# Performance work log

Hardware: AMD Instinct MI355X
Metric: run time of the kernel (lower is better)

## Reference

```python
import jax, jax.numpy as jnp
import numpy as np

B, S, D = 8, 1024, 768
H = 12
HD = D // H  # 64
SCALE = 1.0 / (HD ** 0.5)


def setup_inputs() -> dict:
    key = jax.random.key(0)
    ks = jax.random.split(key, 5)
    x = jax.random.normal(ks[0], (B, S, D), dtype=jnp.float32)
    W_qkv = jax.random.normal(ks[1], (D, 3 * D), dtype=jnp.float32) * 0.02
    b_qkv = jax.random.normal(ks[2], (3 * D,), dtype=jnp.float32) * 0.02
    W_proj = jax.random.normal(ks[3], (D, D), dtype=jnp.float32) * 0.02
    b_proj = jax.random.normal(ks[4], (D,), dtype=jnp.float32) * 0.02
    return {"x": x, "W_qkv": W_qkv, "b_qkv": b_qkv, "W_proj": W_proj, "b_proj": b_proj}


def reference(x, W_qkv, b_qkv, W_proj, b_proj):
    b, s, d = x.shape
    # QKV projection: (B, S, 3D) -> (3, B, H, S, HD)
    qkv = x @ W_qkv + b_qkv
    qkv = qkv.reshape(b, s, 3, H, HD).transpose(2, 0, 3, 1, 4)
    q, k, v = qkv[0], qkv[1], qkv[2]
    # scaled dot-product attention (full matrix, as in the original)
    scores = jnp.einsum("bhqd,bhkd->bhqk", q, k) * SCALE
    attn = jax.nn.softmax(scores, axis=-1)
    out = jnp.einsum("bhqk,bhkd->bhqd", attn, v)
    # merge heads: (B, S, D)
    out = out.transpose(0, 2, 1, 3).reshape(b, s, d)
    return out @ W_proj + b_proj
```

## Files before the change

kernel.cpp:

```cpp
#include <hip/hip_runtime.h>
#include <math.h>

typedef __attribute__((ext_vector_type(8))) unsigned short ushortx8;
typedef __attribute__((ext_vector_type(8))) __bf16 bf16x8;
typedef __attribute__((ext_vector_type(4))) float floatx4;
typedef __attribute__((ext_vector_type(16))) float floatx16;

#define NH 12
#define SEQ 1024
#define DM 768
#define HD 64
#define GK 768
#define QK_SCALE 0.18033688011112042f

#define GLDS16(gp, lp) __builtin_amdgcn_global_load_lds( \
    (const __attribute__((address_space(1))) unsigned int*)(const void*)(gp), \
    (__attribute__((address_space(3))) unsigned int*)(lp), 16, 0, 0)

__device__ __forceinline__ unsigned short f2bf(float f) {
    union { float f; unsigned u; } v; v.f = f;
    unsigned r = v.u + 0x7fffu + ((v.u >> 16) & 1u);
    return (unsigned short)(r >> 16);
}

__device__ __forceinline__ unsigned pk2bf(float f0, float f1) {
    union { float f; unsigned u; } a, b; a.f = f0; b.f = f1;
    return ((a.u + 0x8000u) >> 16) | ((b.u + 0x8000u) & 0xffff0000u);
}

__device__ __forceinline__ float fast_exp2(float x) {
    float r;
    asm("v_exp_f32 %0, %1" : "=v"(r) : "v"(x));
    return r;
}

__global__ void k_prep(const float* __restrict__ x, unsigned short* __restrict__ x_bf,
                       const float* __restrict__ Wqkv, unsigned short* __restrict__ WqkvT,
                       const float* __restrict__ Wproj, unsigned short* __restrict__ WprojT) {
    __shared__ float tile[32][33];
    int bx = blockIdx.x;
    if (bx < 6144) {
        int i = bx * 256 + threadIdx.x;
        float4 v = ((const float4*)x)[i];
        ushort4 o;
        o.x = f2bf(v.x); o.y = f2bf(v.y); o.z = f2bf(v.z); o.w = f2bf(v.w);
        ((ushort4*)x_bf)[i] = o;
        return;
    }
    const float* in; unsigned short* out; int R, C, c0, r0;
    if (bx < 7872) {
        int t = bx - 6144;
        in = Wqkv; out = WqkvT; R = 768; C = 2304;
        c0 = (t % 72) * 32; r0 = (t / 72) * 32;
    } else {
        int t = bx - 7872;
        in = Wproj; out = WprojT; R = 768; C = 768;
        c0 = (t % 24) * 32; r0 = (t / 24) * 32;
    }
    int tx = threadIdx.x & 31, ty = threadIdx.x >> 5;
#pragma unroll
    for (int i = 0; i < 4; i++)
        tile[ty + 8 * i][tx] = in[(size_t)(r0 + ty + 8 * i) * C + c0 + tx];
    __syncthreads();
#pragma unroll
    for (int i = 0; i < 4; i++)
        out[(size_t)(c0 + ty + 8 * i) * R + r0 + tx] = f2bf(tile[tx][ty + 8 * i]);
}

__device__ __forceinline__ void stage6(const unsigned short* gA, const unsigned short* gB,
                                       unsigned short* lbuf, int w, int k0) {
#pragma unroll
    for (int g = 0; g < 4; g++)
        GLDS16(gA + (size_t)(w * 64 + g * 16) * GK + k0, lbuf + (w * 64 + g * 16) * 32);
#pragma unroll
    for (int g = 0; g < 2; g++)
        GLDS16(gB + (size_t)(w * 32 + g * 16) * GK + k0, lbuf + 8192 + (w * 32 + g * 16) * 32);
}

__device__ __forceinline__ void mfma24(const unsigned short* Ab, const unsigned short* Bb,
                                       int wm, int wn, int l15, int csw,
                                       floatx4 (&acc)[8][3]) {
    bf16x8 af[8], bfr[3];
#pragma unroll
    for (int m = 0; m < 8; m++)
        af[m] = __builtin_bit_cast(bf16x8,
            *(const ushortx8*)&Ab[(wm * 128 + m * 16 + l15) * 32 + csw]);
#pragma unroll
    for (int n = 0; n < 3; n++)
        bfr[n] = __builtin_bit_cast(bf16x8,
            *(const ushortx8*)&Bb[(wn * 48 + n * 16 + l15) * 32 + csw]);
#pragma unroll
    for (int m = 0; m < 8; m++)
#pragma unroll
        for (int n = 0; n < 3; n++)
            acc[m][n] = __builtin_amdgcn_mfma_f32_16x16x32_bf16(af[m], bfr[n], acc[m][n], 0, 0, 0);
}

__device__ __forceinline__ void gemm_mainloop(const unsigned short* __restrict__ A,
                                              const unsigned short* __restrict__ Bt,
                                              unsigned short* smem, int m0, int n0,
                                              int w, int lane, floatx4 (&acc)[8][3]) {
    int quad = lane >> 4, l15 = lane & 15;
    int wm = w >> 1, wn = w & 1;
    int rA = lane >> 2;
    int cSwz = ((lane & 3) ^ ((lane >> 3) & 3)) * 8;
    int csw = (quad ^ ((l15 >> 1) & 3)) * 8;
    const unsigned short* gA = A + (size_t)(m0 + rA) * GK + cSwz;
    const unsigned short* gB = Bt + (size_t)(n0 + rA) * GK + cSwz;

    stage6(gA, gB, smem, w, 0);
    stage6(gA, gB, smem + 12288, w, 32);
#pragma unroll 1
    for (int t = 0; t < 24; t++) {
        if (t < 23) asm volatile("s_waitcnt vmcnt(6)" ::: "memory");
        else        asm volatile("s_waitcnt vmcnt(0)" ::: "memory");
        __builtin_amdgcn_s_barrier();
        asm volatile("" ::: "memory");
        const unsigned short* Ab = smem + (t & 1) * 12288;
        __builtin_amdgcn_s_setprio(1);
        mfma24(Ab, Ab + 8192, wm, wn, l15, csw, acc);
        __builtin_amdgcn_s_setprio(0);
        asm volatile("" ::: "memory");
        __builtin_amdgcn_s_barrier();
        asm volatile("" ::: "memory");
        if (t < 22) stage6(gA, gB, smem + (t & 1) * 12288, w, (t + 2) * 32);
    }
}

__global__ __launch_bounds__(256, 3) void k_gemm_qkv(
    const unsigned short* __restrict__ A, const unsigned short* __restrict__ Bt,
    const float* __restrict__ bias,
    unsigned short* __restrict__ Qb, unsigned short* __restrict__ Kb,
    unsigned short* __restrict__ Vt) {
    __shared__ unsigned short smem[25344];
    int tid = threadIdx.x;
    int w = tid >> 6, lane = tid & 63;
    int quad = lane >> 4, l15 = lane & 15;
    int wm = w >> 1, wn = w & 1;
    int lin = blockIdx.x;
    int xcd = lin & 7, slot = lin >> 3;
    int mt_i = xcd * 4 + (slot & 3);
    int nt_i = slot >> 2;
    int m0 = mt_i * 256, n0 = nt_i * 96;

    floatx4 acc[8][3] = {};
    gemm_mainloop(A, Bt, smem, m0, n0, w, lane, acc);

    int tsel = nt_i / 8;
    int bb = m0 >> 10;
    int s_base0 = (m0 & 1023) + wm * 128;
    if (tsel < 2) {
        unsigned short* __restrict__ dst = (tsel == 0) ? Qb : Kb;
#pragma unroll
        for (int m = 0; m < 8; m++) {
            int s_base = s_base0 + m * 16 + quad * 4;
#pragma unroll
            for (int n = 0; n < 3; n++) {
                int n_g = n0 + wn * 48 + n * 16 + l15;
                int nloc = n_g - tsel * 768;
                int hh = nloc >> 6, dd = nloc & 63;
                float bv = bias[n_g];
                size_t base = ((size_t)(bb * NH + hh) * SEQ + s_base) * HD + dd;
                if (tsel == 0) {
#pragma unroll
                    for (int rg = 0; rg < 4; rg++)
                        dst[base + (size_t)rg * HD] = f2bf((acc[m][n][rg] + bv) * QK_SCALE);
                } else {
#pragma unroll
                    for (int rg = 0; rg < 4; rg++)
                        dst[base + (size_t)rg * HD] = f2bf(acc[m][n][rg] + bv);
                }
            }
        }
    } else {
        __syncthreads();
#pragma unroll
        for (int m = 0; m < 8; m++) {
#pragma unroll
            for (int n = 0; n < 3; n++) {
                int col = wn * 48 + n * 16 + l15;
                float bv = bias[n0 + col];
                ushort4 pk;
                pk.x = f2bf(acc[m][n][0] + bv);
                pk.y = f2bf(acc[m][n][1] + bv);
                pk.z = f2bf(acc[m][n][2] + bv);
                pk.w = f2bf(acc[m][n][3] + bv);
                *(ushort4*)&smem[col * 264 + wm * 128 + m * 16 + quad * 4] = pk;
            }
        }
        __syncthreads();
        if (tid < 192) {
            int col = tid >> 1, part = tid & 1;
            int dglob = (n0 - 1536) + col;
            int hh = dglob >> 6, dd = dglob & 63;
            size_t gbase = ((size_t)(bb * NH + hh) * HD + dd) * SEQ + (m0 & 1023) + part * 128;
#pragma unroll
            for (int i = 0; i < 16; i++)
                *(uint4*)&Vt[gbase + i * 8] = *(const uint4*)&smem[col * 264 + part * 128 + i * 8];
        }
    }
}

__global__ __launch_bounds__(256) void k_attn(
    const unsigned short* __restrict__ Qb, const unsigned short* __restrict__ Kb,
    const unsigned short* __restrict__ Vt, unsigned short* __restrict__ attn_out) {
    __shared__ unsigned short Ks[2][64 * 64];
    __shared__ unsigned short Vts[2][64 * 64];
    __shared__ unsigned short Pt[4][32 * 72];
    int tid = threadIdx.x;
    int w = tid >> 6, lane = tid & 63;
    int l31 = lane & 31, lh = lane >> 5;
    int lin = blockIdx.x;
    int xcd = lin & 7, slot = lin >> 3;
    int bh = xcd * 12 + (slot >> 3);
    int qt = slot & 7;
    int b = bh / NH, h = bh - b * NH;
    const unsigned short* Qp = Qb + (size_t)bh * SEQ * HD;
    const unsigned short* Kp = Kb + (size_t)bh * SEQ * HD;
    const unsigned short* Vp = Vt + (size_t)bh * HD * SEQ;
    int q0w = qt * 128 + w * 32;
    unsigned short* Ptw = &Pt[w][0];

    bf16x8 qf[4];
#pragma unroll
    for (int ds = 0; ds < 4; ds++)
        qf[ds] = __builtin_bit_cast(bf16x8,
            *(const ushortx8*)&Qp[(size_t)(q0w + l31) * HD + ds * 16 + lh * 8]);

    floatx16 o[2] = {};
    float lsum = 0.f;

    int rr = tid >> 3, cc8 = (tid & 7) * 8;
    int cs = cc8 ^ ((rr & 7) * 8);
    int rsw = (l31 & 7) * 8;

    {
        uint4 a = *(const uint4*)&Kp[(size_t)rr * HD + cc8];
        uint4 b2 = *(const uint4*)&Kp[(size_t)(rr + 32) * HD + cc8];
        uint4 c = *(const uint4*)&Vp[(size_t)rr * SEQ + cc8];
        uint4 d = *(const uint4*)&Vp[(size_t)(rr + 32) * SEQ + cc8];
        *(uint4*)&Ks[0][rr * 64 + cs] = a;
        *(uint4*)&Ks[0][(rr + 32) * 64 + cs] = b2;
        *(uint4*)&Vts[0][rr * 64 + cs] = c;
        *(uint4*)&Vts[0][(rr + 32) * 64 + cs] = d;
    }
    uint4 kr0 = *(const uint4*)&Kp[(size_t)(64 + rr) * HD + cc8];
    uint4 kr1 = *(const uint4*)&Kp[(size_t)(64 + rr + 32) * HD + cc8];
    uint4 vr0 = *(const uint4*)&Vp[(size_t)rr * SEQ + 64 + cc8];
    uint4 vr1 = *(const uint4*)&Vp[(size_t)(rr + 32) * SEQ + 64 + cc8];
    __syncthreads();

    for (int kb = 0; kb < SEQ; kb += 64) {
        int cur = (kb >> 6) & 1;
        if (kb + 64 < SEQ) {
            *(uint4*)&Ks[cur ^ 1][rr * 64 + cs] = kr0;
            *(uint4*)&Ks[cur ^ 1][(rr + 32) * 64 + cs] = kr1;
            *(uint4*)&Vts[cur ^ 1][rr * 64 + cs] = vr0;
            *(uint4*)&Vts[cur ^ 1][(rr + 32) * 64 + cs] = vr1;
            if (kb + 128 < SEQ) {
                kr0 = *(const uint4*)&Kp[(size_t)(kb + 128 + rr) * HD + cc8];
                kr1 = *(const uint4*)&Kp[(size_t)(kb + 128 + rr + 32) * HD + cc8];
                vr0 = *(const uint4*)&Vp[(size_t)rr * SEQ + kb + 128 + cc8];
                vr1 = *(const uint4*)&Vp[(size_t)(rr + 32) * SEQ + kb + 128 + cc8];
            }
        }

        floatx16 sc[2] = {};
        __builtin_amdgcn_s_setprio(1);
#pragma unroll
        for (int mt = 0; mt < 2; mt++)
#pragma unroll
            for (int ds = 0; ds < 4; ds++) {
                bf16x8 kf = __builtin_bit_cast(bf16x8,
                    *(const ushortx8*)&Ks[cur][(mt * 32 + l31) * 64 + ((ds * 16 + lh * 8) ^ rsw)]);
                sc[mt] = __builtin_amdgcn_mfma_f32_32x32x16_bf16(kf, qf[ds], sc[mt], 0, 0, 0);
            }
        __builtin_amdgcn_s_setprio(0);

        float p0[16], p1[16];
#pragma unroll
        for (int r = 0; r < 16; r++) {
            p0[r] = fast_exp2(sc[0][r]);
            p1[r] = fast_exp2(sc[1][r]);
            lsum += p0[r] + p1[r];
        }

        uint4 pw[4];
#pragma unroll
        for (int mt = 0; mt < 2; mt++) {
            const float* pp = mt ? p1 : p0;
#pragma unroll
            for (int hf = 0; hf < 2; hf++) {
                unsigned a, bq, c, d;
                asm("v_cvt_pk_bf16_f32 %0, %1, %2" : "=v"(a)  : "v"(pp[hf * 8 + 0]), "v"(pp[hf * 8 + 1]));
                asm("v_cvt_pk_bf16_f32 %0, %1, %2" : "=v"(bq) : "v"(pp[hf * 8 + 4]), "v"(pp[hf * 8 + 5]));
                asm("v_cvt_pk_bf16_f32 %0, %1, %2" : "=v"(c)  : "v"(pp[hf * 8 + 2]), "v"(pp[hf * 8 + 3]));
                asm("v_cvt_pk_bf16_f32 %0, %1, %2" : "=v"(d)  : "v"(pp[hf * 8 + 6]), "v"(pp[hf * 8 + 7]));
                asm("v_permlane32_swap_b32 %0, %1" : "+v"(a), "+v"(bq));
                asm("v_permlane32_swap_b32 %0, %1" : "+v"(c), "+v"(d));
                uint4 wv; wv.x = a; wv.y = c; wv.z = bq; wv.w = d;
                pw[mt * 2 + hf] = wv;
            }
        }

        __builtin_amdgcn_s_setprio(1);
#pragma unroll
        for (int ks = 0; ks < 4; ks++) {
            bf16x8 pf = __builtin_bit_cast(bf16x8, pw[ks]);
#pragma unroll
            for (int mt = 0; mt < 2; mt++) {
                bf16x8 vf = __builtin_bit_cast(bf16x8,
                    *(const ushortx8*)&Vts[cur][(mt * 32 + l31) * 64 + ((ks * 16 + lh * 8) ^ rsw)]);
                o[mt] = __builtin_amdgcn_mfma_f32_32x32x16_bf16(vf, pf, o[mt], 0, 0, 0);
            }
        }
        __builtin_amdgcn_s_setprio(0);

        __syncthreads();
    }

    lsum += __shfl_xor(lsum, 32, 64);
    float inv = 1.0f / lsum;

#pragma unroll
    for (int mt = 0; mt < 2; mt++)
#pragma unroll
        for (int g = 0; g < 4; g++) {
            uint2 pk;
            pk.x = pk2bf(o[mt][g * 4 + 0] * inv, o[mt][g * 4 + 1] * inv);
            pk.y = pk2bf(o[mt][g * 4 + 2] * inv, o[mt][g * 4 + 3] * inv);
            *(uint2*)&Ptw[l31 * 72 + mt * 32 + g * 8 + lh * 4] = pk;
        }
    __builtin_amdgcn_s_barrier();
#pragma unroll
    for (int pass = 0; pass < 4; pass++) {
        int row = pass * 8 + (lane >> 3);
        int col8 = (lane & 7) * 8;
        uint4 vv = *(const uint4*)&Ptw[row * 72 + col8];
        *(uint4*)&attn_out[(size_t)(b * SEQ + q0w + row) * DM + h * HD + col8] = vv;
    }
}

__device__ __forceinline__ void stage4(const unsigned short* gA, const unsigned short* gB,
                                       unsigned short* lbuf, int w, int k0) {
#pragma unroll
    for (int g = 0; g < 2; g++)
        GLDS16(gA + (size_t)(w * 32 + g * 16) * GK + k0, lbuf + (w * 32 + g * 16) * 32);
#pragma unroll
    for (int g = 0; g < 2; g++)
        GLDS16(gB + (size_t)(w * 32 + g * 16) * GK + k0, lbuf + 4096 + (w * 32 + g * 16) * 32);
}

__device__ __forceinline__ void mfma12(const unsigned short* Ab, const unsigned short* Bb,
                                       int wm, int wn, int l15, int csw,
                                       floatx4 (&acc)[4][3]) {
    bf16x8 af[4], bfr[3];
#pragma unroll
    for (int m = 0; m < 4; m++)
        af[m] = __builtin_bit_cast(bf16x8,
            *(const ushortx8*)&Ab[(wm * 64 + m * 16 + l15) * 32 + csw]);
#pragma unroll
    for (int n = 0; n < 3; n++)
        bfr[n] = __builtin_bit_cast(bf16x8,
            *(const ushortx8*)&Bb[(wn * 48 + n * 16 + l15) * 32 + csw]);
#pragma unroll
    for (int m = 0; m < 4; m++)
#pragma unroll
        for (int n = 0; n < 3; n++)
            acc[m][n] = __builtin_amdgcn_mfma_f32_16x16x32_bf16(af[m], bfr[n], acc[m][n], 0, 0, 0);
}

__global__ __launch_bounds__(256, 2) void k_gemm_proj(
    const unsigned short* __restrict__ A, const unsigned short* __restrict__ Bt,
    const float* __restrict__ bias, float* __restrict__ out) {
    __shared__ unsigned short smem[16384];
    int tid = threadIdx.x;
    int w = tid >> 6, lane = tid & 63;
    int quad = lane >> 4, l15 = lane & 15;
    int wm = w >> 1, wn = w & 1;
    int lin = blockIdx.x;
    int xcd = lin & 7, slot = lin >> 3;
    int mt_i = xcd * 8 + (slot & 7);
    int nt_i = slot >> 3;
    int m0 = mt_i * 128, n0 = nt_i * 96;

    int rA = lane >> 2;
    int cSwz = ((lane & 3) ^ ((lane >> 3) & 3)) * 8;
    int csw = (quad ^ ((l15 >> 1) & 3)) * 8;
    const unsigned short* gA = A + (size_t)(m0 + rA) * GK + cSwz;
    const unsigned short* gB = Bt + (size_t)(n0 + rA) * GK + cSwz;

    floatx4 acc[4][3] = {};
    stage4(gA, gB, smem, w, 0);
    stage4(gA, gB, smem + 8192, w, 32);
#pragma unroll 1
    for (int t = 0; t < 24; t++) {
        if (t < 23) asm volatile("s_waitcnt vmcnt(4)" ::: "memory");
        else        asm volatile("s_waitcnt vmcnt(0)" ::: "memory");
        __builtin_amdgcn_s_barrier();
        asm volatile("" ::: "memory");
        const unsigned short* Ab = smem + (t & 1) * 8192;
        __builtin_amdgcn_s_setprio(1);
        mfma12(Ab, Ab + 4096, wm, wn, l15, csw, acc);
        __builtin_amdgcn_s_setprio(0);
        asm volatile("" ::: "memory");
        __builtin_amdgcn_s_barrier();
        asm volatile("" ::: "memory");
        if (t < 22) stage4(gA, gB, smem + (t & 1) * 8192, w, (t + 2) * 32);
    }

#pragma unroll
    for (int m = 0; m < 4; m++) {
        int m_base = m0 + wm * 64 + m * 16 + quad * 4;
#pragma unroll
        for (int n = 0; n < 3; n++) {
            int n_g = n0 + wn * 48 + n * 16 + l15;
            float bv = bias[n_g];
#pragma unroll
            for (int rg = 0; rg < 4; rg++)
                out[(size_t)(m_base + rg) * DM + n_g] = acc[m][n][rg] + bv;
        }
    }
}

extern "C" void kernel_launch(void* const* d_in, const int* in_sizes, int n_in,
                              void* d_out, int out_size, void* d_ws, size_t ws_size,
                              hipStream_t stream) {
    const float* x     = (const float*)d_in[0];
    const float* Wqkv  = (const float*)d_in[1];
    const float* bqkv  = (const float*)d_in[2];
    const float* Wproj = (const float*)d_in[3];
    const float* bproj = (const float*)d_in[4];
    float* out = (float*)d_out;

    char* ws = (char*)d_ws;
    unsigned short* x_bf   = (unsigned short*)(ws);
    unsigned short* WqkvT  = (unsigned short*)(ws + 12582912);
    unsigned short* WprojT = (unsigned short*)(ws + 16121856);
    unsigned short* Qb     = (unsigned short*)(ws + 17301504);
    unsigned short* Kb     = (unsigned short*)(ws + 29884416);
    unsigned short* Vt     = (unsigned short*)(ws + 42467328);
    unsigned short* attn   = (unsigned short*)(ws + 55050240);

    k_prep<<<8448, 256, 0, stream>>>(x, x_bf, Wqkv, WqkvT, Wproj, WprojT);
    k_gemm_qkv<<<768, 256, 0, stream>>>(x_bf, WqkvT, bqkv, Qb, Kb, Vt);
    k_attn<<<768, 256, 0, stream>>>(Qb, Kb, Vt, attn);
    k_gemm_proj<<<512, 256, 0, stream>>>(attn, WprojT, bproj, out);
}
```

Baseline: 183.9 us.

## Raise occupancy: alias attention LDS, split sum accumulators, halve proj GEMM tile

The attention kernel now reuses the K/V shared buffers for the output transpose staging instead of a separate Pt array, and declares four blocks per CU. This lowers LDS use per block so more blocks can be resident. The row-sum accumulation is split into four independent partial sums to shorten the dependency chain. The projection GEMM moves from 128-row to 64-row tiles with three loads per stage and twice as many blocks, targeting better occupancy and wave fill at the cost of less B-operand reuse per block.

New measurement: 194.6 us. 5.8% more time.

```diff
diff --git a/kernel.cpp b/kernel.cpp
--- a/kernel.cpp
+++ b/kernel.cpp
@@ -201,12 +201,12 @@
     }
 }
 
-__global__ __launch_bounds__(256) void k_attn(
+__global__ __launch_bounds__(256, 4) void k_attn(
     const unsigned short* __restrict__ Qb, const unsigned short* __restrict__ Kb,
     const unsigned short* __restrict__ Vt, unsigned short* __restrict__ attn_out) {
-    __shared__ unsigned short Ks[2][64 * 64];
-    __shared__ unsigned short Vts[2][64 * 64];
-    __shared__ unsigned short Pt[4][32 * 72];
+    __shared__ unsigned short smem[16384];
+    unsigned short* Ks = smem;
+    unsigned short* Vts = smem + 8192;
     int tid = threadIdx.x;
     int w = tid >> 6, lane = tid & 63;
     int l31 = lane & 31, lh = lane >> 5;
@@ -219,7 +219,6 @@
     const unsigned short* Kp = Kb + (size_t)bh * SEQ * HD;
     const unsigned short* Vp = Vt + (size_t)bh * HD * SEQ;
     int q0w = qt * 128 + w * 32;
-    unsigned short* Ptw = &Pt[w][0];
 
     bf16x8 qf[4];
 #pragma unroll
@@ -228,7 +227,7 @@
             *(const ushortx8*)&Qp[(size_t)(q0w + l31) * HD + ds * 16 + lh * 8]);
 
     floatx16 o[2] = {};
-    float lsum = 0.f;
+    float ls0 = 0.f, ls1 = 0.f, ls2 = 0.f, ls3 = 0.f;
 
     int rr = tid >> 3, cc8 = (tid & 7) * 8;
     int cs = cc8 ^ ((rr & 7) * 8);
@@ -239,10 +238,10 @@
         uint4 b2 = *(const uint4*)&Kp[(size_t)(rr + 32) * HD + cc8];
         uint4 c = *(const uint4*)&Vp[(size_t)rr * SEQ + cc8];
         uint4 d = *(const uint4*)&Vp[(size_t)(rr + 32) * SEQ + cc8];
-        *(uint4*)&Ks[0][rr * 64 + cs] = a;
-        *(uint4*)&Ks[0][(rr + 32) * 64 + cs] = b2;
-        *(uint4*)&Vts[0][rr * 64 + cs] = c;
-        *(uint4*)&Vts[0][(rr + 32) * 64 + cs] = d;
+        *(uint4*)&Ks[rr * 64 + cs] = a;
+        *(uint4*)&Ks[(rr + 32) * 64 + cs] = b2;
+        *(uint4*)&Vts[rr * 64 + cs] = c;
+        *(uint4*)&Vts[(rr + 32) * 64 + cs] = d;
     }
     uint4 kr0 = *(const uint4*)&Kp[(size_t)(64 + rr) * HD + cc8];
     uint4 kr1 = *(const uint4*)&Kp[(size_t)(64 + rr + 32) * HD + cc8];
@@ -253,10 +252,10 @@
     for (int kb = 0; kb < SEQ; kb += 64) {
         int cur = (kb >> 6) & 1;
         if (kb + 64 < SEQ) {
-            *(uint4*)&Ks[cur ^ 1][rr * 64 + cs] = kr0;
-            *(uint4*)&Ks[cur ^ 1][(rr + 32) * 64 + cs] = kr1;
-            *(uint4*)&Vts[cur ^ 1][rr * 64 + cs] = vr0;
-            *(uint4*)&Vts[cur ^ 1][(rr + 32) * 64 + cs] = vr1;
+            *(uint4*)&Ks[(cur ^ 1) * 4096 + rr * 64 + cs] = kr0;
+            *(uint4*)&Ks[(cur ^ 1) * 4096 + (rr + 32) * 64 + cs] = kr1;
+            *(uint4*)&Vts[(cur ^ 1) * 4096 + rr * 64 + cs] = vr0;
+            *(uint4*)&Vts[(cur ^ 1) * 4096 + (rr + 32) * 64 + cs] = vr1;
             if (kb + 128 < SEQ) {
                 kr0 = *(const uint4*)&Kp[(size_t)(kb + 128 + rr) * HD + cc8];
                 kr1 = *(const uint4*)&Kp[(size_t)(kb + 128 + rr + 32) * HD + cc8];
@@ -272,17 +271,22 @@
 #pragma unroll
             for (int ds = 0; ds < 4; ds++) {
                 bf16x8 kf = __builtin_bit_cast(bf16x8,
-                    *(const ushortx8*)&Ks[cur][(mt * 32 + l31) * 64 + ((ds * 16 + lh * 8) ^ rsw)]);
+                    *(const ushortx8*)&Ks[cur * 4096 + (mt * 32 + l31) * 64 + ((ds * 16 + lh * 8) ^ rsw)]);
                 sc[mt] = __builtin_amdgcn_mfma_f32_32x32x16_bf16(kf, qf[ds], sc[mt], 0, 0, 0);
             }
         __builtin_amdgcn_s_setprio(0);
 
         float p0[16], p1[16];
 #pragma unroll
-        for (int r = 0; r < 16; r++) {
-            p0[r] = fast_exp2(sc[0][r]);
-            p1[r] = fast_exp2(sc[1][r]);
-            lsum += p0[r] + p1[r];
+        for (int r = 0; r < 16; r += 4) {
+            p0[r]     = fast_exp2(sc[0][r]);     p1[r]     = fast_exp2(sc[1][r]);
+            p0[r + 1] = fast_exp2(sc[0][r + 1]); p1[r + 1] = fast_exp2(sc[1][r + 1]);
+            p0[r + 2] = fast_exp2(sc[0][r + 2]); p1[r + 2] = fast_exp2(sc[1][r + 2]);
+            p0[r + 3] = fast_exp2(sc[0][r + 3]); p1[r + 3] = fast_exp2(sc[1][r + 3]);
+            ls0 += p0[r]     + p1[r];
+            ls1 += p0[r + 1] + p1[r + 1];
+            ls2 += p0[r + 2] + p1[r + 2];
+            ls3 += p0[r + 3] + p1[r + 3];
         }
 
         uint4 pw[4];
@@ -310,7 +314,7 @@
 #pragma unroll
             for (int mt = 0; mt < 2; mt++) {
                 bf16x8 vf = __builtin_bit_cast(bf16x8,
-                    *(const ushortx8*)&Vts[cur][(mt * 32 + l31) * 64 + ((ks * 16 + lh * 8) ^ rsw)]);
+                    *(const ushortx8*)&Vts[cur * 4096 + (mt * 32 + l31) * 64 + ((ks * 16 + lh * 8) ^ rsw)]);
                 o[mt] = __builtin_amdgcn_mfma_f32_32x32x16_bf16(vf, pf, o[mt], 0, 0, 0);
             }
         }
@@ -319,9 +323,11 @@
         __syncthreads();
     }
 
+    float lsum = (ls0 + ls1) + (ls2 + ls3);
     lsum += __shfl_xor(lsum, 32, 64);
     float inv = 1.0f / lsum;
 
+    unsigned short* Ptw = smem + w * 2304;
 #pragma unroll
     for (int mt = 0; mt < 2; mt++)
 #pragma unroll
@@ -341,48 +347,46 @@
     }
 }
 
-__device__ __forceinline__ void stage4(const unsigned short* gA, const unsigned short* gB,
+__device__ __forceinline__ void stage3(const unsigned short* gA, const unsigned short* gB,
                                        unsigned short* lbuf, int w, int k0) {
+    GLDS16(gA + (size_t)(w * 16) * GK + k0, lbuf + (w * 16) * 32);
 #pragma unroll
     for (int g = 0; g < 2; g++)
-        GLDS16(gA + (size_t)(w * 32 + g * 16) * GK + k0, lbuf + (w * 32 + g * 16) * 32);
-#pragma unroll
-    for (int g = 0; g < 2; g++)
-        GLDS16(gB + (size_t)(w * 32 + g * 16) * GK + k0, lbuf + 4096 + (w * 32 + g * 16) * 32);
-}
-
-__device__ __forceinline__ void mfma12(const unsigned short* Ab, const unsigned short* Bb,
-                                       int wm, int wn, int l15, int csw,
-                                       floatx4 (&acc)[4][3]) {
-    bf16x8 af[4], bfr[3];
-#pragma unroll
-    for (int m = 0; m < 4; m++)
+        GLDS16(gB + (size_t)(w * 32 + g * 16) * GK + k0, lbuf + 2048 + (w * 32 + g * 16) * 32);
+}
+
+__device__ __forceinline__ void mfma6(const unsigned short* Ab, const unsigned short* Bb,
+                                      int wm, int wn, int l15, int csw,
+                                      floatx4 (&acc)[2][3]) {
+    bf16x8 af[2], bfr[3];
+#pragma unroll
+    for (int m = 0; m < 2; m++)
         af[m] = __builtin_bit_cast(bf16x8,
-            *(const ushortx8*)&Ab[(wm * 64 + m * 16 + l15) * 32 + csw]);
+            *(const ushortx8*)&Ab[(wm * 32 + m * 16 + l15) * 32 + csw]);
 #pragma unroll
     for (int n = 0; n < 3; n++)
         bfr[n] = __builtin_bit_cast(bf16x8,
             *(const ushortx8*)&Bb[(wn * 48 + n * 16 + l15) * 32 + csw]);
 #pragma unroll
-    for (int m = 0; m < 4; m++)
+    for (int m = 0; m < 2; m++)
 #pragma unroll
         for (int n = 0; n < 3; n++)
             acc[m][n] = __builtin_amdgcn_mfma_f32_16x16x32_bf16(af[m], bfr[n], acc[m][n], 0, 0, 0);
 }
 
-__global__ __launch_bounds__(256, 2) void k_gemm_proj(
+__global__ __launch_bounds__(256, 4) void k_gemm_proj(
     const unsigned short* __restrict__ A, const unsigned short* __restrict__ Bt,
     const float* __restrict__ bias, float* __restrict__ out) {
-    __shared__ unsigned short smem[16384];
+    __shared__ unsigned short smem[12288];
     int tid = threadIdx.x;
     int w = tid >> 6, lane = tid & 63;
     int quad = lane >> 4, l15 = lane & 15;
     int wm = w >> 1, wn = w & 1;
     int lin = blockIdx.x;
     int xcd = lin & 7, slot = lin >> 3;
-    int mt_i = xcd * 8 + (slot & 7);
-    int nt_i = slot >> 3;
-    int m0 = mt_i * 128, n0 = nt_i * 96;
+    int mt_i = xcd * 16 + (slot & 15);
+    int nt_i = slot >> 4;
+    int m0 = mt_i * 64, n0 = nt_i * 96;
 
     int rA = lane >> 2;
     int cSwz = ((lane & 3) ^ ((lane >> 3) & 3)) * 8;
@@ -390,28 +394,28 @@
     const unsigned short* gA = A + (size_t)(m0 + rA) * GK + cSwz;
     const unsigned short* gB = Bt + (size_t)(n0 + rA) * GK + cSwz;
 
-    floatx4 acc[4][3] = {};
-    stage4(gA, gB, smem, w, 0);
-    stage4(gA, gB, smem + 8192, w, 32);
+    floatx4 acc[2][3] = {};
+    stage3(gA, gB, smem, w, 0);
+    stage3(gA, gB, smem + 6144, w, 32);
 #pragma unroll 1
     for (int t = 0; t < 24; t++) {
-        if (t < 23) asm volatile("s_waitcnt vmcnt(4)" ::: "memory");
+        if (t < 23) asm volatile("s_waitcnt vmcnt(3)" ::: "memory");
         else        asm volatile("s_waitcnt vmcnt(0)" ::: "memory");
         __builtin_amdgcn_s_barrier();
         asm volatile("" ::: "memory");
-        const unsigned short* Ab = smem + (t & 1) * 8192;
+        const unsigned short* Ab = smem + (t & 1) * 6144;
         __builtin_amdgcn_s_setprio(1);
-        mfma12(Ab, Ab + 4096, wm, wn, l15, csw, acc);
+        mfma6(Ab, Ab + 2048, wm, wn, l15, csw, acc);
         __builtin_amdgcn_s_setprio(0);
         asm volatile("" ::: "memory");
         __builtin_amdgcn_s_barrier();
         asm volatile("" ::: "memory");
-        if (t < 22) stage4(gA, gB, smem + (t & 1) * 8192, w, (t + 2) * 32);
-    }
-
-#pragma unroll
-    for (int m = 0; m < 4; m++) {
-        int m_base = m0 + wm * 64 + m * 16 + quad * 4;
+        if (t < 22) stage3(gA, gB, smem + (t & 1) * 6144, w, (t + 2) * 32);
+    }
+
+#pragma unroll
+    for (int m = 0; m < 2; m++) {
+        int m_base = m0 + wm * 32 + m * 16 + quad * 4;
 #pragma unroll
         for (int n = 0; n < 3; n++) {
             int n_g = n0 + wn * 48 + n * 16 + l15;
@@ -445,5 +449,5 @@
     k_prep<<<8448, 256, 0, stream>>>(x, x_bf, Wqkv, WqkvT, Wproj, WprojT);
     k_gemm_qkv<<<768, 256, 0, stream>>>(x_bf, WqkvT, bqkv, Qb, Kb, Vt);
     k_attn<<<768, 256, 0, stream>>>(Qb, Kb, Vt, attn);
-    k_gemm_proj<<<512, 256, 0, stream>>>(attn, WprojT, bproj, out);
-}
+    k_gemm_proj<<<1024, 256, 0, stream>>>(attn, WprojT, bproj, out);
+}
```
